# Performance work log

Hardware: AMD Instinct MI355X
Metric: run time of the kernel (lower is better)

The kernel has to match this reference:

```python
import jax, jax.numpy as jnp
import numpy as np

NUM_HEADS = 16
HEAD_DIM = 128  # 2048 / 16


def setup_inputs() -> dict:
    key = jax.random.key(0)
    ks = jax.random.split(key, 5)
    B, S, D = 2, 2048, 2048
    scale = 1.0 / np.sqrt(D)
    return {
        "x": jax.random.normal(ks[0], (B, S, D), dtype=jnp.float32),
        "Wq": jax.random.normal(ks[1], (D, D), dtype=jnp.float32) * scale,
        "Wk": jax.random.normal(ks[2], (D, D), dtype=jnp.float32) * scale,
        "Wv": jax.random.normal(ks[3], (D, D), dtype=jnp.float32) * scale,
        "Wo": jax.random.normal(ks[4], (D, D), dtype=jnp.float32) * scale,
    }


def reference(x, Wq, Wk, Wv, Wo):
    B, S, D = x.shape
    H, Hd = NUM_HEADS, HEAD_DIM
    # nn.Linear(bias=False): y = x @ W.T
    q = (x @ Wq.T).reshape(B, S, H, Hd).transpose(0, 2, 1, 3)  # [B,H,S,Hd]
    k = (x @ Wk.T).reshape(B, S, H, Hd).transpose(0, 2, 1, 3)
    v = (x @ Wv.T).reshape(B, S, H, Hd).transpose(0, 2, 1, 3)
    scores = jnp.einsum("bhqd,bhkd->bhqk", q, k) / jnp.sqrt(jnp.float32(Hd))
    attn = jax.nn.softmax(scores, axis=-1)  # dropout p=0 (eval) -> identity
    out = jnp.einsum("bhqk,bhkd->bhqd", attn, v)  # [B,H,S,Hd]
    out = out.transpose(0, 2, 1, 3).reshape(B, S, D)
    out = out @ Wo.T
    return out
```

## Files before the change

kernel.cpp:

```cpp
#include <hip/hip_runtime.h>
#include <math.h>
#include <stdint.h>


#define DDIM 2048
#define SEQ  2048
#define NH   16
#define HD   128

typedef __attribute__((ext_vector_type(4))) float f32x4;
typedef __attribute__((ext_vector_type(8))) __bf16 bf16x8;
typedef __attribute__((ext_vector_type(4))) unsigned int u32x4;
typedef __attribute__((ext_vector_type(2))) unsigned int u32x2;

#define MFMA_B16(a, b, c) __builtin_amdgcn_mfma_f32_16x16x32_bf16((a), (b), (c), 0, 0, 0)

__device__ __forceinline__ void async16(const void* g, void* l) {
  __builtin_amdgcn_global_load_lds(
      (const __attribute__((address_space(1))) unsigned int*)g,
      (__attribute__((address_space(3))) unsigned int*)l, 16, 0, 0);
}

__device__ __forceinline__ unsigned short f2bf(float f) {
  unsigned u = __builtin_bit_cast(unsigned, f);
  u += 0x7fffu + ((u >> 16) & 1u);
  return (unsigned short)(u >> 16);
}

__device__ __forceinline__ bf16x8 ldfrag(const unsigned short* p) {
  return __builtin_bit_cast(bf16x8, *(const u32x4*)p);
}

__global__ __launch_bounds__(256) void cvt_bf16_kernel(const float* __restrict__ s,
                                                       unsigned short* __restrict__ d) {
  const int i = blockIdx.x * 256 + threadIdx.x;
  const f32x4* sp = (const f32x4*)s;
  f32x4 a = sp[2 * i], b = sp[2 * i + 1];
  u32x4 o;
  o.x = ((unsigned)f2bf(a.y) << 16) | f2bf(a.x);
  o.y = ((unsigned)f2bf(a.w) << 16) | f2bf(a.z);
  o.z = ((unsigned)f2bf(b.y) << 16) | f2bf(b.x);
  o.w = ((unsigned)f2bf(b.w) << 16) | f2bf(b.z);
  ((u32x4*)d)[i] = o;
}

__global__ __launch_bounds__(256) void gemm_qkv(const unsigned short* __restrict__ A,
                                                const unsigned short* __restrict__ B,
                                                unsigned short* __restrict__ Oqk,
                                                unsigned short* __restrict__ Ovt,
                                                float alpha_q) {
  __shared__ unsigned short As[128 * 64];
  __shared__ unsigned short Bs[128 * 64];
  const int tid = threadIdx.x;
  const int lane = tid & 63, w = tid >> 6;
  const int quad = lane >> 4, l16 = lane & 15;
  const int wm = (w >> 1) * 64, wn = (w & 1) * 64;
  const int bm = blockIdx.y * 128, bn = blockIdx.x * 128;

  f32x4 acc[4][4];
#pragma unroll
  for (int i = 0; i < 4; i++)
#pragma unroll
    for (int j = 0; j < 4; j++) acc[i][j] = f32x4{0.f, 0.f, 0.f, 0.f};

  for (int kt = 0; kt < DDIM / 64; ++kt) {
    __syncthreads();
#pragma unroll
    for (int j = 0; j < 4; ++j) {
      int i8 = j * 256 + tid;
      int row = i8 >> 3, cs = i8 & 7, cg = cs ^ (row & 7);
      size_t go = (size_t)kt * 64 + cg * 8;
      async16(A + (size_t)(bm + row) * DDIM + go, &As[i8 * 8]);
      async16(B + (size_t)(bn + row) * DDIM + go, &Bs[i8 * 8]);
    }
    __syncthreads();
#pragma unroll
    for (int ks = 0; ks < 2; ++ks) {
      bf16x8 af[4], bfv[4];
#pragma unroll
      for (int t = 0; t < 4; ++t) {
        int sl = (ks * 4 + quad) ^ (l16 & 7);
        af[t] = ldfrag(&As[(wm + t * 16 + l16) * 64 + sl * 8]);
        bfv[t] = ldfrag(&Bs[(wn + t * 16 + l16) * 64 + sl * 8]);
      }
#pragma unroll
      for (int i = 0; i < 4; ++i)
#pragma unroll
        for (int j = 0; j < 4; ++j) acc[i][j] = MFMA_B16(af[i], bfv[j], acc[i][j]);
    }
  }

  const int seg = bn >> 11;
  const int bnl = bn & 2047;
  const float alpha = (seg == 0) ? alpha_q : 1.0f;
#pragma unroll
  for (int i = 0; i < 4; ++i) {
    const int mg0 = bm + wm + i * 16 + quad * 4;
#pragma unroll
    for (int j = 0; j < 4; ++j) {
      const int ngl = bnl + wn + j * 16 + l16;
      f32x4 v = acc[i][j] * alpha;
      if (seg < 2) {
        unsigned short* O = Oqk + (size_t)seg * (4096u * 2048u);
        O[(size_t)(mg0 + 0) * DDIM + ngl] = f2bf(v.x);
        O[(size_t)(mg0 + 1) * DDIM + ngl] = f2bf(v.y);
        O[(size_t)(mg0 + 2) * DDIM + ngl] = f2bf(v.z);
        O[(size_t)(mg0 + 3) * DDIM + ngl] = f2bf(v.w);
      } else {
        const int bb = mg0 >> 11, s0 = mg0 & 2047;
        const int hh = ngl >> 7, dd = ngl & 127;
        u32x2 st;
        st.x = ((unsigned)f2bf(v.y) << 16) | f2bf(v.x);
        st.y = ((unsigned)f2bf(v.w) << 16) | f2bf(v.z);
        *(u32x2*)&Ovt[((size_t)((bb * NH + hh) * HD + dd)) * SEQ + s0] = st;
      }
    }
  }
}

__global__ __launch_bounds__(256) void gemm_o(const unsigned short* __restrict__ A,
                                              const unsigned short* __restrict__ B,
                                              float* __restrict__ Cout) {
  __shared__ unsigned short As[128 * 64];
  __shared__ unsigned short Bs[128 * 64];
  const int tid = threadIdx.x;
  const int lane = tid & 63, w = tid >> 6;
  const int quad = lane >> 4, l16 = lane & 15;
  const int wm = (w >> 1) * 64, wn = (w & 1) * 64;
  const int bm = blockIdx.y * 128, bn = blockIdx.x * 128;

  f32x4 acc[4][4];
#pragma unroll
  for (int i = 0; i < 4; i++)
#pragma unroll
    for (int j = 0; j < 4; j++) acc[i][j] = f32x4{0.f, 0.f, 0.f, 0.f};

  for (int kt = 0; kt < DDIM / 64; ++kt) {
    __syncthreads();
#pragma unroll
    for (int j = 0; j < 4; ++j) {
      int i8 = j * 256 + tid;
      int row = i8 >> 3, cs = i8 & 7, cg = cs ^ (row & 7);
      size_t go = (size_t)kt * 64 + cg * 8;
      async16(A + (size_t)(bm + row) * DDIM + go, &As[i8 * 8]);
      async16(B + (size_t)(bn + row) * DDIM + go, &Bs[i8 * 8]);
    }
    __syncthreads();
#pragma unroll
    for (int ks = 0; ks < 2; ++ks) {
      bf16x8 af[4], bfv[4];
#pragma unroll
      for (int t = 0; t < 4; ++t) {
        int sl = (ks * 4 + quad) ^ (l16 & 7);
        af[t] = ldfrag(&As[(wm + t * 16 + l16) * 64 + sl * 8]);
        bfv[t] = ldfrag(&Bs[(wn + t * 16 + l16) * 64 + sl * 8]);
      }
#pragma unroll
      for (int i = 0; i < 4; ++i)
#pragma unroll
        for (int j = 0; j < 4; ++j) acc[i][j] = MFMA_B16(af[i], bfv[j], acc[i][j]);
    }
  }

#pragma unroll
  for (int i = 0; i < 4; ++i) {
    const int mg0 = bm + wm + i * 16 + quad * 4;
#pragma unroll
    for (int j = 0; j < 4; ++j) {
      const int ng = bn + wn + j * 16 + l16;
      f32x4 v = acc[i][j];
      Cout[(size_t)(mg0 + 0) * DDIM + ng] = v.x;
      Cout[(size_t)(mg0 + 1) * DDIM + ng] = v.y;
      Cout[(size_t)(mg0 + 2) * DDIM + ng] = v.z;
      Cout[(size_t)(mg0 + 3) * DDIM + ng] = v.w;
    }
  }
}

__global__ __launch_bounds__(256) void attn_kernel(const unsigned short* __restrict__ qb,
                                                   const unsigned short* __restrict__ kb,
                                                   const unsigned short* __restrict__ vtb,
                                                   unsigned short* __restrict__ ab) {
  __shared__ unsigned short Ks[64 * 128];
  __shared__ unsigned short Vts[128 * 64];
  __shared__ unsigned short Pw[4 * 16 * 40];
  const int tid = threadIdx.x;
  const int w = tid >> 6, lane = tid & 63;
  const int quad = lane >> 4, l16 = lane & 15;
  const int qt = blockIdx.x, bh = blockIdx.y;
  const int b = bh >> 4, h = bh & 15;
  const int qrow = qt * 64 + w * 16 + l16;

  const unsigned short* qp = qb + ((size_t)(b * SEQ + qrow)) * DDIM + h * HD;
  bf16x8 qf[4];
#pragma unroll
  for (int ks = 0; ks < 4; ++ks) qf[ks] = ldfrag(qp + ks * 32 + quad * 8);

  f32x4 ot[8];
#pragma unroll
  for (int i = 0; i < 8; i++) ot[i] = f32x4{0.f, 0.f, 0.f, 0.f};
  float sumacc = 0.f;

  const size_t kbase = ((size_t)(b * SEQ)) * DDIM + h * HD;
  const size_t vbase = ((size_t)((b * NH + h) * HD)) * SEQ;
  unsigned short* pw = &Pw[w * 640];

  for (int kt = 0; kt < SEQ / 64; ++kt) {
    __syncthreads();
#pragma unroll
    for (int j = 0; j < 4; ++j) {
      int i8 = j * 256 + tid;
      int key = i8 >> 4, cs = i8 & 15, cg = cs ^ (key & 15);
      async16(kb + kbase + (size_t)(kt * 64 + key) * DDIM + cg * 8, &Ks[i8 * 8]);
    }
#pragma unroll
    for (int j = 0; j < 4; ++j) {
      int i8 = j * 256 + tid;
      int dd = i8 >> 3, cs = i8 & 7, cg = cs ^ (dd & 7);
      async16(vtb + vbase + (size_t)dd * SEQ + kt * 64 + cg * 8, &Vts[i8 * 8]);
    }
    __syncthreads();
#pragma unroll
    for (int c = 0; c < 2; ++c) {
      f32x4 s0 = {0.f, 0.f, 0.f, 0.f}, s1 = {0.f, 0.f, 0.f, 0.f};
#pragma unroll
      for (int ks = 0; ks < 4; ++ks) {
        int slot = (ks * 4 + quad) ^ l16;
        bf16x8 a0 = ldfrag(&Ks[(c * 32 + l16) * 128 + slot * 8]);
        bf16x8 a1 = ldfrag(&Ks[(c * 32 + 16 + l16) * 128 + slot * 8]);
        s0 = MFMA_B16(a0, qf[ks], s0);
        s1 = MFMA_B16(a1, qf[ks], s1);
      }
      f32x4 p0, p1;
      p0.x = exp2f(s0.x); p0.y = exp2f(s0.y); p0.z = exp2f(s0.z); p0.w = exp2f(s0.w);
      p1.x = exp2f(s1.x); p1.y = exp2f(s1.y); p1.z = exp2f(s1.z); p1.w = exp2f(s1.w);
      sumacc += (p0.x + p0.y + p0.z + p0.w) + (p1.x + p1.y + p1.z + p1.w);
      u32x2 w0, w1;
      w0.x = ((unsigned)f2bf(p0.y) << 16) | f2bf(p0.x);
      w0.y = ((unsigned)f2bf(p0.w) << 16) | f2bf(p0.z);
      w1.x = ((unsigned)f2bf(p1.y) << 16) | f2bf(p1.x);
      w1.y = ((unsigned)f2bf(p1.w) << 16) | f2bf(p1.z);
      *(u32x2*)&pw[l16 * 40 + quad * 4] = w0;
      *(u32x2*)&pw[l16 * 40 + 16 + quad * 4] = w1;
      asm volatile("s_waitcnt lgkmcnt(0)" ::: "memory");
      bf16x8 pb = ldfrag(&pw[l16 * 40 + quad * 8]);
#pragma unroll
      for (int mt = 0; mt < 8; ++mt) {
        int slot = (c * 4 + quad) ^ (l16 & 7);
        bf16x8 vf = ldfrag(&Vts[(mt * 16 + l16) * 64 + slot * 8]);
        ot[mt] = MFMA_B16(vf, pb, ot[mt]);
      }
    }
  }
  float total = sumacc;
  total += __shfl_xor(total, 16);
  total += __shfl_xor(total, 32);
  const float inv = 1.0f / total;
  unsigned short* op = ab + ((size_t)(b * SEQ + qrow)) * DDIM + h * HD;
#pragma unroll
  for (int mt = 0; mt < 8; ++mt) {
    f32x4 v = ot[mt] * inv;
    u32x2 st;
    st.x = ((unsigned)f2bf(v.y) << 16) | f2bf(v.x);
    st.y = ((unsigned)f2bf(v.w) << 16) | f2bf(v.z);
    *(u32x2*)&op[mt * 16 + quad * 4] = st;
  }
}

extern "C" void kernel_launch(void* const* d_in, const int* in_sizes, int n_in,
                              void* d_out, int out_size, void* d_ws, size_t ws_size,
                              hipStream_t stream) {
  (void)in_sizes; (void)n_in; (void)out_size; (void)ws_size;
  const float* x = (const float*)d_in[0];
  const float* Wq = (const float*)d_in[1];
  const float* Wk = (const float*)d_in[2];
  const float* Wv = (const float*)d_in[3];
  const float* Wo = (const float*)d_in[4];

  char* ws = (char*)d_ws;
  unsigned short* xb = (unsigned short*)(ws);
  unsigned short* wqkv = (unsigned short*)(ws + 16777216);
  unsigned short* wkb = (unsigned short*)(ws + 25165824);
  unsigned short* wvb = (unsigned short*)(ws + 33554432);
  unsigned short* qb = (unsigned short*)(ws + 41943040);
  unsigned short* kb = (unsigned short*)(ws + 58720256);
  unsigned short* vtb = (unsigned short*)(ws + 75497472);

  const float alpha_q = 1.44269504088896341f / sqrtf(128.0f);

  cvt_bf16_kernel<<<dim3(4096), 256, 0, stream>>>(x, xb);
  cvt_bf16_kernel<<<dim3(2048), 256, 0, stream>>>(Wq, wqkv);
  cvt_bf16_kernel<<<dim3(2048), 256, 0, stream>>>(Wk, wkb);
  cvt_bf16_kernel<<<dim3(2048), 256, 0, stream>>>(Wv, wvb);

  gemm_qkv<<<dim3(48, 32), 256, 0, stream>>>(xb, wqkv, qb, vtb, alpha_q);
  cvt_bf16_kernel<<<dim3(2048), 256, 0, stream>>>(Wo, wqkv);

  attn_kernel<<<dim3(32, 32), 256, 0, stream>>>(qb, kb, vtb, xb);

  gemm_o<<<dim3(16, 32), 256, 0, stream>>>(xb, wqkv, (float*)d_out);
}
```

Baseline: 418.3 us.

## Use 32x32 MFMA in GEMMs, fuse conversions, restructure attention key loop

The QKV and output GEMMs become a single template built on the 32x32x16 bf16 MFMA, which cuts LDS fragment loads per MFMA, and their global load addresses are precomputed as incrementing pointers. The four fp32-to-bf16 conversion launches merge into one launch. The attention kernel now computes all four 16-key score tiles per 64-key block before doing exp and the PV MFMAs, uses the hardware exp2 builtin, and steps its K/V load pointers incrementally. These changes target MFMA issue efficiency, address arithmetic and launch overhead, at the cost of more registers per thread and a different accumulator store pattern.

```diff
diff --git a/kernel.cpp b/kernel.cpp
--- a/kernel.cpp
+++ b/kernel.cpp
@@ -9,11 +9,13 @@
 #define HD   128
 
 typedef __attribute__((ext_vector_type(4))) float f32x4;
+typedef __attribute__((ext_vector_type(16))) float f32x16;
 typedef __attribute__((ext_vector_type(8))) __bf16 bf16x8;
 typedef __attribute__((ext_vector_type(4))) unsigned int u32x4;
 typedef __attribute__((ext_vector_type(2))) unsigned int u32x2;
 
 #define MFMA_B16(a, b, c) __builtin_amdgcn_mfma_f32_16x16x32_bf16((a), (b), (c), 0, 0, 0)
+#define MFMA32(a, b, c) __builtin_amdgcn_mfma_f32_32x32x16_bf16((a), (b), (c), 0, 0, 0)
 
 __device__ __forceinline__ void async16(const void* g, void* l) {
   __builtin_amdgcn_global_load_lds(
@@ -31,9 +33,8 @@
   return __builtin_bit_cast(bf16x8, *(const u32x4*)p);
 }
 
-__global__ __launch_bounds__(256) void cvt_bf16_kernel(const float* __restrict__ s,
-                                                       unsigned short* __restrict__ d) {
-  const int i = blockIdx.x * 256 + threadIdx.x;
+__device__ __forceinline__ void cvt_body(const float* __restrict__ s,
+                                         unsigned short* __restrict__ d, int i) {
   const f32x4* sp = (const f32x4*)s;
   f32x4 a = sp[2 * i], b = sp[2 * i + 1];
   u32x4 o;
@@ -44,135 +45,123 @@
   ((u32x4*)d)[i] = o;
 }
 
-__global__ __launch_bounds__(256) void gemm_qkv(const unsigned short* __restrict__ A,
-                                                const unsigned short* __restrict__ B,
-                                                unsigned short* __restrict__ Oqk,
-                                                unsigned short* __restrict__ Ovt,
-                                                float alpha_q) {
+__global__ __launch_bounds__(256) void cvt_bf16_kernel(const float* __restrict__ s,
+                                                       unsigned short* __restrict__ d) {
+  cvt_body(s, d, blockIdx.x * 256 + threadIdx.x);
+}
+
+__global__ __launch_bounds__(256) void cvt_all_kernel(const float* __restrict__ x,
+                                                      const float* __restrict__ wq,
+                                                      const float* __restrict__ wk,
+                                                      const float* __restrict__ wv,
+                                                      unsigned short* __restrict__ xb,
+                                                      unsigned short* __restrict__ wqkv) {
+  const int b = blockIdx.x;
+  if (b < 4096) {
+    cvt_body(x, xb, b * 256 + threadIdx.x);
+  } else {
+    const int wi = (b - 4096) >> 11, lb = (b - 4096) & 2047;
+    const float* s = (wi == 0) ? wq : (wi == 1) ? wk : wv;
+    cvt_body(s, wqkv + (size_t)wi * 4194304u, lb * 256 + threadIdx.x);
+  }
+}
+
+template <int MODE>
+__global__ __launch_bounds__(256) void gemm32(const unsigned short* __restrict__ A,
+                                              const unsigned short* __restrict__ B,
+                                              unsigned short* __restrict__ Oqk,
+                                              unsigned short* __restrict__ Ovt,
+                                              float* __restrict__ Cf, float alpha_q) {
   __shared__ unsigned short As[128 * 64];
   __shared__ unsigned short Bs[128 * 64];
   const int tid = threadIdx.x;
   const int lane = tid & 63, w = tid >> 6;
-  const int quad = lane >> 4, l16 = lane & 15;
+  const int l32 = lane & 31, half = lane >> 5;
   const int wm = (w >> 1) * 64, wn = (w & 1) * 64;
   const int bm = blockIdx.y * 128, bn = blockIdx.x * 128;
 
-  f32x4 acc[4][4];
-#pragma unroll
-  for (int i = 0; i < 4; i++)
-#pragma unroll
-    for (int j = 0; j < 4; j++) acc[i][j] = f32x4{0.f, 0.f, 0.f, 0.f};
+  f32x16 acc[2][2];
+#pragma unroll
+  for (int i = 0; i < 2; ++i)
+#pragma unroll
+    for (int j = 0; j < 2; ++j)
+#pragma unroll
+      for (int e = 0; e < 16; ++e) acc[i][j][e] = 0.f;
+
+  const unsigned short* pa[4];
+  const unsigned short* pbb[4];
+  {
+    const int cg = (tid & 7) ^ ((tid >> 3) & 7);
+#pragma unroll
+    for (int j = 0; j < 4; ++j) {
+      const int row = j * 32 + (tid >> 3);
+      pa[j] = A + (size_t)(bm + row) * DDIM + cg * 8;
+      pbb[j] = B + (size_t)(bn + row) * DDIM + cg * 8;
+    }
+  }
 
   for (int kt = 0; kt < DDIM / 64; ++kt) {
     __syncthreads();
 #pragma unroll
     for (int j = 0; j < 4; ++j) {
-      int i8 = j * 256 + tid;
-      int row = i8 >> 3, cs = i8 & 7, cg = cs ^ (row & 7);
-      size_t go = (size_t)kt * 64 + cg * 8;
-      async16(A + (size_t)(bm + row) * DDIM + go, &As[i8 * 8]);
-      async16(B + (size_t)(bn + row) * DDIM + go, &Bs[i8 * 8]);
+      async16(pa[j], &As[(j * 256 + tid) * 8]);
+      pa[j] += 64;
+      async16(pbb[j], &Bs[(j * 256 + tid) * 8]);
+      pbb[j] += 64;
     }
     __syncthreads();
 #pragma unroll
-    for (int ks = 0; ks < 2; ++ks) {
-      bf16x8 af[4], bfv[4];
-#pragma unroll
-      for (int t = 0; t < 4; ++t) {
-        int sl = (ks * 4 + quad) ^ (l16 & 7);
-        af[t] = ldfrag(&As[(wm + t * 16 + l16) * 64 + sl * 8]);
-        bfv[t] = ldfrag(&Bs[(wn + t * 16 + l16) * 64 + sl * 8]);
+    for (int ks = 0; ks < 4; ++ks) {
+      const int sl = ((ks * 2 + half) ^ (l32 & 7)) * 8;
+      bf16x8 af0 = ldfrag(&As[(wm + l32) * 64 + sl]);
+      bf16x8 af1 = ldfrag(&As[(wm + 32 + l32) * 64 + sl]);
+      bf16x8 bf0 = ldfrag(&Bs[(wn + l32) * 64 + sl]);
+      bf16x8 bf1 = ldfrag(&Bs[(wn + 32 + l32) * 64 + sl]);
+      acc[0][0] = MFMA32(af0, bf0, acc[0][0]);
+      acc[0][1] = MFMA32(af0, bf1, acc[0][1]);
+      acc[1][0] = MFMA32(af1, bf0, acc[1][0]);
+      acc[1][1] = MFMA32(af1, bf1, acc[1][1]);
+    }
+  }
+
+  const int seg = (MODE == 0) ? (bn >> 11) : 0;
+  const int bnl = bn & 2047;
+  const float alpha = (MODE == 0 && seg == 0) ? alpha_q : 1.0f;
+#pragma unroll
+  for (int i = 0; i < 2; ++i) {
+#pragma unroll
+    for (int j = 0; j < 2; ++j) {
+#pragma unroll
+      for (int rg = 0; rg < 4; ++rg) {
+        const int m0 = bm + wm + i * 32 + rg * 8 + half * 4;
+        const float v0 = acc[i][j][rg * 4 + 0] * alpha;
+        const float v1 = acc[i][j][rg * 4 + 1] * alpha;
+        const float v2 = acc[i][j][rg * 4 + 2] * alpha;
+        const float v3 = acc[i][j][rg * 4 + 3] * alpha;
+        if (MODE == 1) {
+          const int n = bn + wn + j * 32 + l32;
+          Cf[(size_t)(m0 + 0) * DDIM + n] = v0;
+          Cf[(size_t)(m0 + 1) * DDIM + n] = v1;
+          Cf[(size_t)(m0 + 2) * DDIM + n] = v2;
+          Cf[(size_t)(m0 + 3) * DDIM + n] = v3;
+        } else {
+          const int n = bnl + wn + j * 32 + l32;
+          if (seg < 2) {
+            unsigned short* O = Oqk + (size_t)seg * (4096u * 2048u);
+            O[(size_t)(m0 + 0) * DDIM + n] = f2bf(v0);
+            O[(size_t)(m0 + 1) * DDIM + n] = f2bf(v1);
+            O[(size_t)(m0 + 2) * DDIM + n] = f2bf(v2);
+            O[(size_t)(m0 + 3) * DDIM + n] = f2bf(v3);
+          } else {
+            const int bb = m0 >> 11, s0 = m0 & 2047;
+            const int hh = n >> 7, dd = n & 127;
+            u32x2 st;
+            st.x = ((unsigned)f2bf(v1) << 16) | f2bf(v0);
+            st.y = ((unsigned)f2bf(v3) << 16) | f2bf(v2);
+            *(u32x2*)&Ovt[((size_t)((bb * NH + hh) * HD + dd)) * SEQ + s0] = st;
+          }
+        }
       }
-#pragma unroll
-      for (int i = 0; i < 4; ++i)
-#pragma unroll
-        for (int j = 0; j < 4; ++j) acc[i][j] = MFMA_B16(af[i], bfv[j], acc[i][j]);
-    }
-  }
-
-  const int seg = bn >> 11;
-  const int bnl = bn & 2047;
-  const float alpha = (seg == 0) ? alpha_q : 1.0f;
-#pragma unroll
-  for (int i = 0; i < 4; ++i) {
-    const int mg0 = bm + wm + i * 16 + quad * 4;
-#pragma unroll
-    for (int j = 0; j < 4; ++j) {
-      const int ngl = bnl + wn + j * 16 + l16;
-      f32x4 v = acc[i][j] * alpha;
-      if (seg < 2) {
-        unsigned short* O = Oqk + (size_t)seg * (4096u * 2048u);
-        O[(size_t)(mg0 + 0) * DDIM + ngl] = f2bf(v.x);
-        O[(size_t)(mg0 + 1) * DDIM + ngl] = f2bf(v.y);
-        O[(size_t)(mg0 + 2) * DDIM + ngl] = f2bf(v.z);
-        O[(size_t)(mg0 + 3) * DDIM + ngl] = f2bf(v.w);
-      } else {
-        const int bb = mg0 >> 11, s0 = mg0 & 2047;
-        const int hh = ngl >> 7, dd = ngl & 127;
-        u32x2 st;
-        st.x = ((unsigned)f2bf(v.y) << 16) | f2bf(v.x);
-        st.y = ((unsigned)f2bf(v.w) << 16) | f2bf(v.z);
-        *(u32x2*)&Ovt[((size_t)((bb * NH + hh) * HD + dd)) * SEQ + s0] = st;
-      }
-    }
-  }
-}
-
-__global__ __launch_bounds__(256) void gemm_o(const unsigned short* __restrict__ A,
-                                              const unsigned short* __restrict__ B,
-                                              float* __restrict__ Cout) {
-  __shared__ unsigned short As[128 * 64];
-  __shared__ unsigned short Bs[128 * 64];
-  const int tid = threadIdx.x;
-  const int lane = tid & 63, w = tid >> 6;
-  const int quad = lane >> 4, l16 = lane & 15;
-  const int wm = (w >> 1) * 64, wn = (w & 1) * 64;
-  const int bm = blockIdx.y * 128, bn = blockIdx.x * 128;
-
-  f32x4 acc[4][4];
-#pragma unroll
-  for (int i = 0; i < 4; i++)
-#pragma unroll
-    for (int j = 0; j < 4; j++) acc[i][j] = f32x4{0.f, 0.f, 0.f, 0.f};
-
-  for (int kt = 0; kt < DDIM / 64; ++kt) {
-    __syncthreads();
-#pragma unroll
-    for (int j = 0; j < 4; ++j) {
-      int i8 = j * 256 + tid;
-      int row = i8 >> 3, cs = i8 & 7, cg = cs ^ (row & 7);
-      size_t go = (size_t)kt * 64 + cg * 8;
-      async16(A + (size_t)(bm + row) * DDIM + go, &As[i8 * 8]);
-      async16(B + (size_t)(bn + row) * DDIM + go, &Bs[i8 * 8]);
-    }
-    __syncthreads();
-#pragma unroll
-    for (int ks = 0; ks < 2; ++ks) {
-      bf16x8 af[4], bfv[4];
-#pragma unroll
-      for (int t = 0; t < 4; ++t) {
-        int sl = (ks * 4 + quad) ^ (l16 & 7);
-        af[t] = ldfrag(&As[(wm + t * 16 + l16) * 64 + sl * 8]);
-        bfv[t] = ldfrag(&Bs[(wn + t * 16 + l16) * 64 + sl * 8]);
-      }
-#pragma unroll
-      for (int i = 0; i < 4; ++i)
-#pragma unroll
-        for (int j = 0; j < 4; ++j) acc[i][j] = MFMA_B16(af[i], bfv[j], acc[i][j]);
-    }
-  }
-
-#pragma unroll
-  for (int i = 0; i < 4; ++i) {
-    const int mg0 = bm + wm + i * 16 + quad * 4;
-#pragma unroll
-    for (int j = 0; j < 4; ++j) {
-      const int ng = bn + wn + j * 16 + l16;
-      f32x4 v = acc[i][j];
-      Cout[(size_t)(mg0 + 0) * DDIM + ng] = v.x;
-      Cout[(size_t)(mg0 + 1) * DDIM + ng] = v.y;
-      Cout[(size_t)(mg0 + 2) * DDIM + ng] = v.z;
-      Cout[(size_t)(mg0 + 3) * DDIM + ng] = v.w;
     }
   }
 }
@@ -201,55 +190,78 @@
   for (int i = 0; i < 8; i++) ot[i] = f32x4{0.f, 0.f, 0.f, 0.f};
   float sumacc = 0.f;
 
-  const size_t kbase = ((size_t)(b * SEQ)) * DDIM + h * HD;
-  const size_t vbase = ((size_t)((b * NH + h) * HD)) * SEQ;
+  const unsigned short* kp[4];
+  const unsigned short* vp[4];
+  {
+    const size_t kbase = ((size_t)(b * SEQ)) * DDIM + h * HD;
+    const size_t vbase = ((size_t)((b * NH + h) * HD)) * SEQ;
+#pragma unroll
+    for (int j = 0; j < 4; ++j) {
+      const int key = j * 16 + (tid >> 4), cgk = (tid & 15) ^ (key & 15);
+      kp[j] = kb + kbase + (size_t)key * DDIM + cgk * 8;
+      const int dd = j * 32 + (tid >> 3), cgv = (tid & 7) ^ ((tid >> 3) & 7);
+      vp[j] = vtb + vbase + (size_t)dd * SEQ + cgv * 8;
+    }
+  }
   unsigned short* pw = &Pw[w * 640];
 
   for (int kt = 0; kt < SEQ / 64; ++kt) {
     __syncthreads();
 #pragma unroll
     for (int j = 0; j < 4; ++j) {
-      int i8 = j * 256 + tid;
-      int key = i8 >> 4, cs = i8 & 15, cg = cs ^ (key & 15);
-      async16(kb + kbase + (size_t)(kt * 64 + key) * DDIM + cg * 8, &Ks[i8 * 8]);
-    }
-#pragma unroll
-    for (int j = 0; j < 4; ++j) {
-      int i8 = j * 256 + tid;
-      int dd = i8 >> 3, cs = i8 & 7, cg = cs ^ (dd & 7);
-      async16(vtb + vbase + (size_t)dd * SEQ + kt * 64 + cg * 8, &Vts[i8 * 8]);
+      async16(kp[j], &Ks[(j * 256 + tid) * 8]);
+      kp[j] += (size_t)64 * DDIM;
+      async16(vp[j], &Vts[(j * 256 + tid) * 8]);
+      vp[j] += 64;
     }
     __syncthreads();
-#pragma unroll
-    for (int c = 0; c < 2; ++c) {
-      f32x4 s0 = {0.f, 0.f, 0.f, 0.f}, s1 = {0.f, 0.f, 0.f, 0.f};
-#pragma unroll
-      for (int ks = 0; ks < 4; ++ks) {
-        int slot = (ks * 4 + quad) ^ l16;
-        bf16x8 a0 = ldfrag(&Ks[(c * 32 + l16) * 128 + slot * 8]);
-        bf16x8 a1 = ldfrag(&Ks[(c * 32 + 16 + l16) * 128 + slot * 8]);
-        s0 = MFMA_B16(a0, qf[ks], s0);
-        s1 = MFMA_B16(a1, qf[ks], s1);
+    f32x4 s[4];
+#pragma unroll
+    for (int t = 0; t < 4; ++t) s[t] = f32x4{0.f, 0.f, 0.f, 0.f};
+#pragma unroll
+    for (int ks = 0; ks < 4; ++ks) {
+      const int sl = ((ks * 4 + quad) ^ l16) * 8;
+#pragma unroll
+      for (int t = 0; t < 4; ++t) {
+        bf16x8 a = ldfrag(&Ks[(t * 16 + l16) * 128 + sl]);
+        s[t] = MFMA_B16(a, qf[ks], s[t]);
       }
-      f32x4 p0, p1;
-      p0.x = exp2f(s0.x); p0.y = exp2f(s0.y); p0.z = exp2f(s0.z); p0.w = exp2f(s0.w);
-      p1.x = exp2f(s1.x); p1.y = exp2f(s1.y); p1.z = exp2f(s1.z); p1.w = exp2f(s1.w);
-      sumacc += (p0.x + p0.y + p0.z + p0.w) + (p1.x + p1.y + p1.z + p1.w);
+    }
+    f32x4 p[4];
+#pragma unroll
+    for (int t = 0; t < 4; ++t) {
+      p[t].x = __builtin_amdgcn_exp2f(s[t].x);
+      p[t].y = __builtin_amdgcn_exp2f(s[t].y);
+      p[t].z = __builtin_amdgcn_exp2f(s[t].z);
+      p[t].w = __builtin_amdgcn_exp2f(s[t].w);
+      sumacc += (p[t].x + p[t].y) + (p[t].z + p[t].w);
+    }
+    bf16x8 pb0, pb1;
+    {
       u32x2 w0, w1;
-      w0.x = ((unsigned)f2bf(p0.y) << 16) | f2bf(p0.x);
-      w0.y = ((unsigned)f2bf(p0.w) << 16) | f2bf(p0.z);
-      w1.x = ((unsigned)f2bf(p1.y) << 16) | f2bf(p1.x);
-      w1.y = ((unsigned)f2bf(p1.w) << 16) | f2bf(p1.z);
+      w0.x = ((unsigned)f2bf(p[0].y) << 16) | f2bf(p[0].x);
+      w0.y = ((unsigned)f2bf(p[0].w) << 16) | f2bf(p[0].z);
+      w1.x = ((unsigned)f2bf(p[1].y) << 16) | f2bf(p[1].x);
+      w1.y = ((unsigned)f2bf(p[1].w) << 16) | f2bf(p[1].z);
       *(u32x2*)&pw[l16 * 40 + quad * 4] = w0;
       *(u32x2*)&pw[l16 * 40 + 16 + quad * 4] = w1;
       asm volatile("s_waitcnt lgkmcnt(0)" ::: "memory");
-      bf16x8 pb = ldfrag(&pw[l16 * 40 + quad * 8]);
-#pragma unroll
-      for (int mt = 0; mt < 8; ++mt) {
-        int slot = (c * 4 + quad) ^ (l16 & 7);
-        bf16x8 vf = ldfrag(&Vts[(mt * 16 + l16) * 64 + slot * 8]);
-        ot[mt] = MFMA_B16(vf, pb, ot[mt]);
-      }
+      pb0 = ldfrag(&pw[l16 * 40 + quad * 8]);
+      w0.x = ((unsigned)f2bf(p[2].y) << 16) | f2bf(p[2].x);
+      w0.y = ((unsigned)f2bf(p[2].w) << 16) | f2bf(p[2].z);
+      w1.x = ((unsigned)f2bf(p[3].y) << 16) | f2bf(p[3].x);
+      w1.y = ((unsigned)f2bf(p[3].w) << 16) | f2bf(p[3].z);
+      *(u32x2*)&pw[l16 * 40 + quad * 4] = w0;
+      *(u32x2*)&pw[l16 * 40 + 16 + quad * 4] = w1;
+      asm volatile("s_waitcnt lgkmcnt(0)" ::: "memory");
+      pb1 = ldfrag(&pw[l16 * 40 + quad * 8]);
+    }
+#pragma unroll
+    for (int mt = 0; mt < 8; ++mt) {
+      bf16x8 vf0 = ldfrag(&Vts[(mt * 16 + l16) * 64 + (quad ^ (l16 & 7)) * 8]);
+      ot[mt] = MFMA_B16(vf0, pb0, ot[mt]);
+      bf16x8 vf1 = ldfrag(&Vts[(mt * 16 + l16) * 64 + ((4 + quad) ^ (l16 & 7)) * 8]);
+      ot[mt] = MFMA_B16(vf1, pb1, ot[mt]);
     }
   }
   float total = sumacc;
@@ -280,23 +292,19 @@
   char* ws = (char*)d_ws;
   unsigned short* xb = (unsigned short*)(ws);
   unsigned short* wqkv = (unsigned short*)(ws + 16777216);
-  unsigned short* wkb = (unsigned short*)(ws + 25165824);
-  unsigned short* wvb = (unsigned short*)(ws + 33554432);
   unsigned short* qb = (unsigned short*)(ws + 41943040);
   unsigned short* kb = (unsigned short*)(ws + 58720256);
   unsigned short* vtb = (unsigned short*)(ws + 75497472);
 
   const float alpha_q = 1.44269504088896341f / sqrtf(128.0f);
 
-  cvt_bf16_kernel<<<dim3(4096), 256, 0, stream>>>(x, xb);
-  cvt_bf16_kernel<<<dim3(2048), 256, 0, stream>>>(Wq, wqkv);
-  cvt_bf16_kernel<<<dim3(2048), 256, 0, stream>>>(Wk, wkb);
-  cvt_bf16_kernel<<<dim3(2048), 256, 0, stream>>>(Wv, wvb);
-
-  gemm_qkv<<<dim3(48, 32), 256, 0, stream>>>(xb, wqkv, qb, vtb, alpha_q);
+  cvt_all_kernel<<<dim3(10240), 256, 0, stream>>>(x, Wq, Wk, Wv, xb, wqkv);
+
+  gemm32<0><<<dim3(48, 32), 256, 0, stream>>>(xb, wqkv, qb, vtb, nullptr, alpha_q);
   cvt_bf16_kernel<<<dim3(2048), 256, 0, stream>>>(Wo, wqkv);
 
   attn_kernel<<<dim3(32, 32), 256, 0, stream>>>(qb, kb, vtb, xb);
 
-  gemm_o<<<dim3(16, 32), 256, 0, stream>>>(xb, wqkv, (float*)d_out);
-}
+  gemm32<1><<<dim3(16, 32), 256, 0, stream>>>(xb, wqkv, nullptr, nullptr, (float*)d_out,
+                                              1.0f);
+}
```

Result: faster. 397.3 us (-5.0%).
